# Kernel tuning notes

Hardware: AMD Instinct MI355X
Metric: run time of the kernel (lower is better)

## Reference

```python
import jax, jax.numpy as jnp
import numpy as np

SCALE_BASE = 512.0
GAMMA = 0.96875


def _rotate_every_two(x):
    x1 = x[..., ::2]
    x2 = x[..., 1::2]
    return jnp.stack([-x2, x1], axis=-1).reshape(x.shape)


def _dup_interleave(m):
    # [L, d/2] -> [L, d], each column duplicated: (a,b) -> (a,a,b,b)
    return jnp.repeat(m, 2, axis=-1)


def _xpos(x, downscale=False):
    # x: [B, L, d]; offset = 0 (parallel form)
    B, L, d = x.shape
    half = d // 2
    pos = jnp.arange(L, dtype=x.dtype)
    # xpos per-channel scale base
    sv = (jnp.arange(0, d, 2, dtype=x.dtype) + 0.4 * d) / (1.4 * d)   # [d/2]
    scale = sv[None, :] ** (pos[:, None] / SCALE_BASE)                 # [L, d/2]
    if downscale:
        scale = 1.0 / scale
    inv_freq = 1.0 / (10000.0 ** (jnp.arange(half, dtype=x.dtype) / half))
    sinusoid = pos[:, None] * inv_freq[None, :]                        # [L, d/2]
    sin = _dup_interleave(jnp.sin(sinusoid) * scale)                   # [L, d]
    cos = _dup_interleave(jnp.cos(sinusoid) * scale)                   # [L, d]
    return x * cos[None] + _rotate_every_two(x) * sin[None]


def _get_D(seq_len, dtype):
    idx = jnp.arange(seq_len)
    diff = idx[:, None] - idx[None, :]                                 # n - m
    safe = jnp.where(diff >= 0, diff, 0).astype(dtype)
    return jnp.where(diff >= 0, GAMMA ** safe, jnp.zeros((), dtype))   # [L, L]


def setup_inputs() -> dict:
    key = jax.random.key(0)
    k1, k2, k3, k4 = jax.random.split(key, 4)
    B, L, H, D = 2, 4096, 1024, 64
    X = jax.random.normal(k1, (B, L, H), dtype=jnp.float32)
    W_Q = jax.random.normal(k2, (H, D), dtype=jnp.float32) / H
    W_K = jax.random.normal(k3, (H, D), dtype=jnp.float32) / H
    W_V = jax.random.normal(k4, (H, D), dtype=jnp.float32) / H
    return {"X": X, "W_Q": W_Q, "W_K": W_K, "W_V": W_V}


def reference(X, W_Q, W_K, W_V):
    L = X.shape[1]
    Dmask = _get_D(L, X.dtype)                     # [L, L]
    Q = _xpos(X @ W_Q)                             # [B, L, d]
    K = _xpos(X @ W_K, downscale=True)             # [B, L, d]
    V = X @ W_V                                    # [B, L, v]
    ret = jnp.einsum('bnd,bmd->bnm', Q, K) * Dmask[None]  # [B, L, L]
    return ret @ V                                 # [B, L, v]
```

## Files before the change

### kernel.cpp

```cpp
#include <hip/hip_runtime.h>
#include <math.h>

#define NB 2
#define LL 4096
#define HH 1024
#define DD 64
#define CHK 64
#define NCH 64
#define BLROWS (NB*LL)
#define GAMMA 0.96875f

typedef _Float16 f16x8 __attribute__((ext_vector_type(8)));
typedef float    f32x4 __attribute__((ext_vector_type(4)));

#define WCH 12288

__global__ __launch_bounds__(256) void prep_w(
    const float* __restrict__ WQ, const float* __restrict__ WK,
    const float* __restrict__ WV, _Float16* __restrict__ Whg,
    _Float16* __restrict__ Wlg)
{
    const int g  = blockIdx.x * 256 + threadIdx.x;
    const int m  = g >> 14;
    const int km = g & 16383;
    const int k  = km >> 4;
    const int d4 = (km & 15) * 4;
    const float* Wm = (m == 0) ? WQ : (m == 1) ? WK : WV;
    const float4 w = *(const float4*)&Wm[(size_t)k * DD + d4];
    const float vals[4] = {w.x, w.y, w.z, w.w};
#pragma unroll
    for (int e = 0; e < 4; ++e) {
        const int n = m * 64 + d4 + e;
        const float x = vals[e] * 1024.f;
        const _Float16 h = (_Float16)x;
        const _Float16 l = (_Float16)(x - (float)h);
        const int off = (k >> 6) * WCH +
                        (((n >> 4) * 2 + ((k >> 5) & 1)) * 64 +
                         ((k >> 3) & 3) * 16 + (n & 15)) * 8 + (k & 7);
        Whg[off] = h;
        Wlg[off] = l;
    }
}

__global__ __launch_bounds__(256) void proj_mfma(
    const float* __restrict__ X, const _Float16* __restrict__ Whg,
    const _Float16* __restrict__ Wlg, float* __restrict__ Qx,
    float* __restrict__ Kx, float* __restrict__ Vx)
{
    __shared__ __align__(16) _Float16 lds[28672];
    _Float16* Xh = lds;
    _Float16* Xl = lds + 2048;
    _Float16* Wh = lds + 4096;
    _Float16* Wl = lds + 16384;

    const int tid  = threadIdx.x;
    const int wv   = tid >> 6;
    const int lane = tid & 63;
    const int r0   = blockIdx.x * 32;

    const int xrow = tid >> 3;
    const int xk8  = (tid & 7) * 8;
    const int xslot = (((xrow >> 4) * 2 + (xk8 >> 5)) * 64 +
                       ((xk8 >> 3) & 3) * 16 + (xrow & 15)) * 8;

    f32x4 acc[6];
#pragma unroll
    for (int i = 0; i < 6; ++i) acc[i] = (f32x4){0.f, 0.f, 0.f, 0.f};

    float4 pxa, pxb;
    f16x8  pwh[6], pwl[6];
    {
        const float* xp = &X[(size_t)(r0 + xrow) * HH + xk8];
        pxa = *(const float4*)&xp[0];
        pxb = *(const float4*)&xp[4];
#pragma unroll
        for (int i = 0; i < 6; ++i) {
            pwh[i] = *(const f16x8*)&Whg[(size_t)(tid + i * 256) * 8];
            pwl[i] = *(const f16x8*)&Wlg[(size_t)(tid + i * 256) * 8];
        }
    }

    for (int ch = 0; ch < 16; ++ch) {
        __syncthreads();
        {
            const float xv[8] = {pxa.x, pxa.y, pxa.z, pxa.w,
                                 pxb.x, pxb.y, pxb.z, pxb.w};
            f16x8 hv, lv;
#pragma unroll
            for (int e = 0; e < 8; ++e) {
                const _Float16 h = (_Float16)xv[e];
                hv[e] = h;
                lv[e] = (_Float16)(xv[e] - (float)h);
            }
            *(f16x8*)&Xh[xslot] = hv;
            *(f16x8*)&Xl[xslot] = lv;
#pragma unroll
            for (int i = 0; i < 6; ++i) {
                *(f16x8*)&Wh[(tid + i * 256) * 8] = pwh[i];
                *(f16x8*)&Wl[(tid + i * 256) * 8] = pwl[i];
            }
        }
        __syncthreads();
        if (ch + 1 < 16) {
            const float* xp = &X[(size_t)(r0 + xrow) * HH + (ch + 1) * 64 + xk8];
            pxa = *(const float4*)&xp[0];
            pxb = *(const float4*)&xp[4];
            const size_t cb = (size_t)(ch + 1) * WCH;
#pragma unroll
            for (int i = 0; i < 6; ++i) {
                pwh[i] = *(const f16x8*)&Whg[cb + (size_t)(tid + i * 256) * 8];
                pwl[i] = *(const f16x8*)&Wlg[cb + (size_t)(tid + i * 256) * 8];
            }
        }
#pragma unroll
        for (int kt = 0; kt < 2; ++kt) {
            const f16x8 a0h = *(const f16x8*)&Xh[((0 * 2 + kt) * 64 + lane) * 8];
            const f16x8 a0l = *(const f16x8*)&Xl[((0 * 2 + kt) * 64 + lane) * 8];
            const f16x8 a1h = *(const f16x8*)&Xh[((1 * 2 + kt) * 64 + lane) * 8];
            const f16x8 a1l = *(const f16x8*)&Xl[((1 * 2 + kt) * 64 + lane) * 8];
#pragma unroll
            for (int cj = 0; cj < 3; ++cj) {
                const int ctg = wv * 3 + cj;
                const f16x8 bh = *(const f16x8*)&Wh[((ctg * 2 + kt) * 64 + lane) * 8];
                const f16x8 bl = *(const f16x8*)&Wl[((ctg * 2 + kt) * 64 + lane) * 8];
                acc[cj] = __builtin_amdgcn_mfma_f32_16x16x32_f16(a0h, bh, acc[cj], 0, 0, 0);
                acc[cj] = __builtin_amdgcn_mfma_f32_16x16x32_f16(a0h, bl, acc[cj], 0, 0, 0);
                acc[cj] = __builtin_amdgcn_mfma_f32_16x16x32_f16(a0l, bh, acc[cj], 0, 0, 0);
                acc[3 + cj] = __builtin_amdgcn_mfma_f32_16x16x32_f16(a1h, bh, acc[3 + cj], 0, 0, 0);
                acc[3 + cj] = __builtin_amdgcn_mfma_f32_16x16x32_f16(a1h, bl, acc[3 + cj], 0, 0, 0);
                acc[3 + cj] = __builtin_amdgcn_mfma_f32_16x16x32_f16(a1l, bh, acc[3 + cj], 0, 0, 0);
            }
        }
    }

    const int quad = lane >> 4;
    const int c16  = lane & 15;
#pragma unroll
    for (int rt = 0; rt < 2; ++rt) {
#pragma unroll
        for (int cj = 0; cj < 3; ++cj) {
            const int ctg = wv * 3 + cj;
            const f32x4 v = acc[rt * 3 + cj];
            const int col = ctg * 16 + c16;
            const int mat = ctg >> 2;
            const int d   = col & 63;
            if (mat < 2) {
                const int i2 = d >> 1;
                const float sv   = (2.f * (float)i2 + 25.6f) / 89.6f;
                const float l2sv = log2f(sv);
                const float ifr  = exp2f(-13.28771237954945f * ((float)i2 / 32.f));
                const float sgn  = (mat == 0) ? 1.f : -1.f;
                float* dst = (mat == 0) ? Qx : Kx;
#pragma unroll
                for (int r = 0; r < 4; ++r) {
                    const int row = r0 + rt * 16 + quad * 4 + r;
                    const float val = v[r] * (1.f / 1024.f);
                    const float p = __shfl_xor(val, 1, 64);
                    const float pf = (float)(row & (LL - 1));
                    const float scl = exp2f(sgn * (pf * (1.f / 512.f)) * l2sv);
                    float s, c;
                    sincosf(pf * ifr, &s, &c);
                    s *= scl; c *= scl;
                    const float o = ((col & 1) == 0) ? val * c - p * s
                                                     : val * c + p * s;
                    dst[(size_t)row * DD + d] = o;
                }
            } else {
#pragma unroll
                for (int r = 0; r < 4; ++r) {
                    const int row = r0 + rt * 16 + quad * 4 + r;
                    Vx[(size_t)row * DD + d] = v[r] * (1.f / 1024.f);
                }
            }
        }
    }
}

__global__ __launch_bounds__(256) void chunk_kv(
    const float* __restrict__ Kx, const float* __restrict__ Vx,
    float* __restrict__ U)
{
    __shared__ float Kl[CHK][DD];
    __shared__ float Vl[CHK][32];
    const int tid   = threadIdx.x;
    const int bc    = blockIdx.x;
    const int chunk = bc >> 1;
    const int dph   = (bc & 1) * 32;
    const size_t base = (size_t)chunk * CHK * DD;
    const float l2g = log2f(GAMMA);
#pragma unroll
    for (int i = 0; i < 4; ++i) {
        const int f   = tid + i * 256;
        const int row = f >> 4;
        const int c4  = (f & 15) * 4;
        float4 kv = *(const float4*)&Kx[base + (size_t)row * DD + c4];
        const float w = exp2f((float)(CHK - 1 - row) * l2g);
        kv.x *= w; kv.y *= w; kv.z *= w; kv.w *= w;
        *(float4*)&Kl[row][c4] = kv;
    }
#pragma unroll
    for (int i = 0; i < 2; ++i) {
        const int f   = tid + i * 256;
        const int row = f >> 3;
        const int c4  = (f & 7) * 4;
        *(float4*)&Vl[row][c4] = *(const float4*)&Vx[base + (size_t)row * DD + dph + c4];
    }
    __syncthreads();
    const int dgr = tid >> 4;
    const int dc  = tid & 15;
    float a[4][2] = {{0,0},{0,0},{0,0},{0,0}};
#pragma unroll 8
    for (int j = 0; j < CHK; ++j) {
        const float4 kv = *(const float4*)&Kl[j][dgr * 4];
        const float2 vv = *(const float2*)&Vl[j][dc * 2];
        a[0][0] += kv.x * vv.x; a[0][1] += kv.x * vv.y;
        a[1][0] += kv.y * vv.x; a[1][1] += kv.y * vv.y;
        a[2][0] += kv.z * vv.x; a[2][1] += kv.z * vv.y;
        a[3][0] += kv.w * vv.x; a[3][1] += kv.w * vv.y;
    }
#pragma unroll
    for (int r = 0; r < 4; ++r) {
        *(float2*)&U[((size_t)chunk * DD + dgr * 4 + r) * DD + dph + dc * 2] =
            make_float2(a[r][0], a[r][1]);
    }
}

__global__ __launch_bounds__(256) void chunk_out(
    const float* __restrict__ Qx, const float* __restrict__ Kx,
    const float* __restrict__ Vx, const float* __restrict__ U,
    float* __restrict__ out)
{
    __shared__ __align__(16) float smA[6272];
    __shared__ __align__(16) float VTl[128 * 64];
    __shared__ float pwl[CHK + 1];
    const int tid   = threadIdx.x;
    const int bc    = blockIdx.x;
    const int chunk = bc >> 1;
    const int nh    = (bc & 1) * 32;
    const size_t base = (size_t)chunk * CHK * DD;

    if (tid <= CHK) pwl[tid] = exp2f((float)tid * log2f(GAMMA));

#pragma unroll
    for (int i = 0; i < 2; ++i) {
        const int f   = tid + i * 256;
        const int row = f >> 4;
        const int c4  = (f & 15) * 4;
        *(float4*)&smA[row * 68 + c4] =
            *(const float4*)&Qx[base + (size_t)(nh + row) * DD + c4];
    }
#pragma unroll
    for (int i = 0; i < 4; ++i) {
        const int f  = tid + i * 256;
        const int m  = f & 63;
        const int k4 = (f >> 6) * 4;
        const float4 kk = *(const float4*)&Kx[base + (size_t)m * DD + k4];
        smA[2176 + (k4 + 0) * 64 + m] = kk.x;
        smA[2176 + (k4 + 1) * 64 + m] = kk.y;
        smA[2176 + (k4 + 2) * 64 + m] = kk.z;
        smA[2176 + (k4 + 3) * 64 + m] = kk.w;
    }
#pragma unroll
    for (int i = 0; i < 4; ++i) {
        const int f   = tid + i * 256;
        const int row = f >> 4;
        const int c4  = (f & 15) * 4;
        *(float4*)&VTl[row * 64 + c4] =
            *(const float4*)&Vx[base + (size_t)row * DD + c4];
    }
    {
        const int cloc = chunk & 63;
        const float g64 = exp2f(64.f * log2f(GAMMA));
#pragma unroll
        for (int i = 0; i < 4; ++i) {
            const int f   = tid + i * 256;
            const int row = f >> 4;
            const int c4  = (f & 15) * 4;
            float tx = 0.f, ty = 0.f, tz = 0.f, tw = 0.f;
            float w = 1.f;
            for (int dl = 1; dl <= 8; ++dl) {
                if (dl <= cloc) {
                    const float4 u = *(const float4*)
                        &U[((size_t)(chunk - dl) * DD + row) * DD + c4];
                    tx += w * u.x; ty += w * u.y; tz += w * u.z; tw += w * u.w;
                }
                w *= g64;
            }
            *(float4*)&VTl[(64 + row) * 64 + c4] = make_float4(tx, ty, tz, tw);
        }
    }
    __syncthreads();

    const int ng = tid >> 4;
    const int mg = tid & 15;
    const int m0 = mg * 4;
    float sacc[2][4];
#pragma unroll
    for (int r = 0; r < 2; ++r)
#pragma unroll
        for (int j = 0; j < 4; ++j) sacc[r][j] = 0.f;

#pragma unroll 4
    for (int k4 = 0; k4 < 16; ++k4) {
        const float4 qv0 = *(const float4*)&smA[(ng * 2 + 0) * 68 + k4 * 4];
        const float4 qv1 = *(const float4*)&smA[(ng * 2 + 1) * 68 + k4 * 4];
#pragma unroll
        for (int u = 0; u < 4; ++u) {
            const float4 kv = *(const float4*)&smA[2176 + (k4 * 4 + u) * 64 + m0];
            const float x0 = (u == 0) ? qv0.x : (u == 1) ? qv0.y : (u == 2) ? qv0.z : qv0.w;
            const float x1 = (u == 0) ? qv1.x : (u == 1) ? qv1.y : (u == 2) ? qv1.z : qv1.w;
            sacc[0][0] += x0 * kv.x; sacc[0][1] += x0 * kv.y; sacc[0][2] += x0 * kv.z; sacc[0][3] += x0 * kv.w;
            sacc[1][0] += x1 * kv.x; sacc[1][1] += x1 * kv.y; sacc[1][2] += x1 * kv.z; sacc[1][3] += x1 * kv.w;
        }
    }
    const float4 qa0 = *(const float4*)&smA[(ng * 2 + 0) * 68 + m0];
    const float4 qa1 = *(const float4*)&smA[(ng * 2 + 1) * 68 + m0];
    __syncthreads();

#pragma unroll
    for (int r = 0; r < 2; ++r) {
        const int nl = ng * 2 + r;
        const int n  = nh + nl;
        float4 sv;
        sv.x = (n >= m0 + 0) ? sacc[r][0] * pwl[n - (m0 + 0)] : 0.f;
        sv.y = (n >= m0 + 1) ? sacc[r][1] * pwl[n - (m0 + 1)] : 0.f;
        sv.z = (n >= m0 + 2) ? sacc[r][2] * pwl[n - (m0 + 2)] : 0.f;
        sv.w = (n >= m0 + 3) ? sacc[r][3] * pwl[n - (m0 + 3)] : 0.f;
        *(float4*)&smA[nl * 132 + m0] = sv;
        const float w = pwl[n + 1];
        const float4 qa = r ? qa1 : qa0;
        *(float4*)&smA[nl * 132 + 64 + m0] =
            make_float4(qa.x * w, qa.y * w, qa.z * w, qa.w * w);
    }
    __syncthreads();

    const int dg = tid & 15;
    float oacc[2][4];
#pragma unroll
    for (int r = 0; r < 2; ++r)
#pragma unroll
        for (int j = 0; j < 4; ++j) oacc[r][j] = 0.f;

#pragma unroll 4
    for (int m4 = 0; m4 < 32; ++m4) {
        const float4 s0 = *(const float4*)&smA[(ng * 2 + 0) * 132 + m4 * 4];
        const float4 s1 = *(const float4*)&smA[(ng * 2 + 1) * 132 + m4 * 4];
#pragma unroll
        for (int mm = 0; mm < 4; ++mm) {
            const float4 vv = *(const float4*)&VTl[(m4 * 4 + mm) * 64 + dg * 4];
            const float a0 = (mm == 0) ? s0.x : (mm == 1) ? s0.y : (mm == 2) ? s0.z : s0.w;
            const float a1 = (mm == 0) ? s1.x : (mm == 1) ? s1.y : (mm == 2) ? s1.z : s1.w;
            oacc[0][0] += a0 * vv.x; oacc[0][1] += a0 * vv.y; oacc[0][2] += a0 * vv.z; oacc[0][3] += a0 * vv.w;
            oacc[1][0] += a1 * vv.x; oacc[1][1] += a1 * vv.y; oacc[1][2] += a1 * vv.z; oacc[1][3] += a1 * vv.w;
        }
    }
#pragma unroll
    for (int r = 0; r < 2; ++r) {
        *(float4*)&out[base + (size_t)(nh + ng * 2 + r) * DD + dg * 4] =
            make_float4(oacc[r][0], oacc[r][1], oacc[r][2], oacc[r][3]);
    }
}

extern "C" void kernel_launch(void* const* d_in, const int* in_sizes, int n_in,
                              void* d_out, int out_size, void* d_ws, size_t ws_size,
                              hipStream_t stream)
{
    const float* X  = (const float*)d_in[0];
    const float* WQ = (const float*)d_in[1];
    const float* WK = (const float*)d_in[2];
    const float* WV = (const float*)d_in[3];
    float* out = (float*)d_out;

    float* ws = (float*)d_ws;
    float* Qx = ws;
    float* Kx = Qx + (size_t)BLROWS * DD;
    float* Vx = Kx + (size_t)BLROWS * DD;
    float* U  = Vx + (size_t)BLROWS * DD;
    _Float16* Whg = (_Float16*)(U + (size_t)NB * NCH * DD * DD);
    _Float16* Wlg = Whg + 196608;

    hipLaunchKernelGGL(prep_w, dim3(192), dim3(256), 0, stream,
                       WQ, WK, WV, Whg, Wlg);
    hipLaunchKernelGGL(proj_mfma, dim3(BLROWS / 32), dim3(256), 0, stream,
                       X, Whg, Wlg, Qx, Kx, Vx);
    hipLaunchKernelGGL(chunk_kv, dim3(2 * NB * NCH), dim3(256), 0, stream, Kx, Vx, U);
    hipLaunchKernelGGL(chunk_out, dim3(2 * NB * NCH), dim3(256), 0, stream,
                       Qx, Kx, Vx, U, out);
}
```

Baseline: 124.3 us.

## Store Q/K/V as fp16 with chunk-relative xpos scaling and MFMA chunk attention

Projections now write Q, K and V in fp16, and the xpos scale is taken relative to the row's position inside its 64-row chunk, with the inter-chunk scale folded into the state-combination factors. This halves intermediate traffic and avoids fp16 overflow. A new prep_vt kernel combines the decayed U states and lays out V and the state into MFMA B-fragment order. chunk_out now uses fp16 MFMA for both QK^T and SV instead of scalar FMA. The weight prep writes directly in fragment order with vector stores. The changes add an extra launch and lower precision, which risks tolerance failures.

```diff
diff --git a/kernel.cpp b/kernel.cpp
--- a/kernel.cpp
+++ b/kernel.cpp
@@ -8,9 +8,11 @@
 #define CHK 64
 #define NCH 64
 #define BLROWS (NB*LL)
+#define NCHT (NB*NCH)
 #define GAMMA 0.96875f
 
 typedef _Float16 f16x8 __attribute__((ext_vector_type(8)));
+typedef _Float16 f16x4 __attribute__((ext_vector_type(4)));
 typedef float    f32x4 __attribute__((ext_vector_type(4)));
 
 #define WCH 12288
@@ -20,32 +22,35 @@
     const float* __restrict__ WV, _Float16* __restrict__ Whg,
     _Float16* __restrict__ Wlg)
 {
-    const int g  = blockIdx.x * 256 + threadIdx.x;
-    const int m  = g >> 14;
-    const int km = g & 16383;
-    const int k  = km >> 4;
-    const int d4 = (km & 15) * 4;
+    const unsigned t = blockIdx.x * 256 + threadIdx.x;
+    const unsigned kchunk = t / 1536u;
+    const unsigned s = t - kchunk * 1536u;
+    const int ct2  = s >> 6;
+    const int lane = s & 63;
+    const int n16  = ct2 >> 1;
+    const int kt   = ct2 & 1;
+    const int quad = lane >> 4;
+    const int n    = n16 * 16 + (lane & 15);
+    const int k0   = (int)kchunk * 64 + kt * 32 + quad * 8;
+    const int m    = n >> 6;
+    const int d    = n & 63;
     const float* Wm = (m == 0) ? WQ : (m == 1) ? WK : WV;
-    const float4 w = *(const float4*)&Wm[(size_t)k * DD + d4];
-    const float vals[4] = {w.x, w.y, w.z, w.w};
-#pragma unroll
-    for (int e = 0; e < 4; ++e) {
-        const int n = m * 64 + d4 + e;
-        const float x = vals[e] * 1024.f;
+    f16x8 hv, lv;
+#pragma unroll
+    for (int j = 0; j < 8; ++j) {
+        const float x = Wm[(size_t)(k0 + j) * DD + d] * 1024.f;
         const _Float16 h = (_Float16)x;
-        const _Float16 l = (_Float16)(x - (float)h);
-        const int off = (k >> 6) * WCH +
-                        (((n >> 4) * 2 + ((k >> 5) & 1)) * 64 +
-                         ((k >> 3) & 3) * 16 + (n & 15)) * 8 + (k & 7);
-        Whg[off] = h;
-        Wlg[off] = l;
-    }
+        hv[j] = h;
+        lv[j] = (_Float16)(x - (float)h);
+    }
+    *(f16x8*)&Whg[(size_t)t * 8] = hv;
+    *(f16x8*)&Wlg[(size_t)t * 8] = lv;
 }
 
 __global__ __launch_bounds__(256) void proj_mfma(
     const float* __restrict__ X, const _Float16* __restrict__ Whg,
-    const _Float16* __restrict__ Wlg, float* __restrict__ Qx,
-    float* __restrict__ Kx, float* __restrict__ Vx)
+    const _Float16* __restrict__ Wlg, _Float16* __restrict__ Qr,
+    _Float16* __restrict__ Kr, _Float16* __restrict__ Vr)
 {
     __shared__ __align__(16) _Float16 lds[28672];
     _Float16* Xh = lds;
@@ -150,26 +155,27 @@
                 const float l2sv = log2f(sv);
                 const float ifr  = exp2f(-13.28771237954945f * ((float)i2 / 32.f));
                 const float sgn  = (mat == 0) ? 1.f : -1.f;
-                float* dst = (mat == 0) ? Qx : Kx;
+                _Float16* dst = (mat == 0) ? Qr : Kr;
 #pragma unroll
                 for (int r = 0; r < 4; ++r) {
                     const int row = r0 + rt * 16 + quad * 4 + r;
                     const float val = v[r] * (1.f / 1024.f);
                     const float p = __shfl_xor(val, 1, 64);
-                    const float pf = (float)(row & (LL - 1));
-                    const float scl = exp2f(sgn * (pf * (1.f / 512.f)) * l2sv);
+                    const float pf  = (float)(row & (LL - 1));
+                    const float pfs = (float)(row & 63);
+                    const float scl = exp2f(sgn * (pfs * (1.f / 512.f)) * l2sv);
                     float s, c;
                     sincosf(pf * ifr, &s, &c);
                     s *= scl; c *= scl;
                     const float o = ((col & 1) == 0) ? val * c - p * s
                                                      : val * c + p * s;
-                    dst[(size_t)row * DD + d] = o;
+                    dst[(size_t)row * DD + d] = (_Float16)o;
                 }
             } else {
 #pragma unroll
                 for (int r = 0; r < 4; ++r) {
                     const int row = r0 + rt * 16 + quad * 4 + r;
-                    Vx[(size_t)row * DD + d] = v[r] * (1.f / 1024.f);
+                    Vr[(size_t)row * DD + d] = (_Float16)(v[r] * (1.f / 1024.f));
                 }
             }
         }
@@ -177,33 +183,27 @@
 }
 
 __global__ __launch_bounds__(256) void chunk_kv(
-    const float* __restrict__ Kx, const float* __restrict__ Vx,
+    const _Float16* __restrict__ Kr, const _Float16* __restrict__ Vr,
     float* __restrict__ U)
 {
-    __shared__ float Kl[CHK][DD];
-    __shared__ float Vl[CHK][32];
+    __shared__ _Float16 Kl[64 * 64];
+    __shared__ _Float16 Vl[64 * 32];
+    __shared__ float pwd[64];
     const int tid   = threadIdx.x;
     const int bc    = blockIdx.x;
     const int chunk = bc >> 1;
     const int dph   = (bc & 1) * 32;
-    const size_t base = (size_t)chunk * CHK * DD;
+    const size_t rbase = (size_t)chunk * CHK * DD;
     const float l2g = log2f(GAMMA);
-#pragma unroll
-    for (int i = 0; i < 4; ++i) {
-        const int f   = tid + i * 256;
-        const int row = f >> 4;
-        const int c4  = (f & 15) * 4;
-        float4 kv = *(const float4*)&Kx[base + (size_t)row * DD + c4];
-        const float w = exp2f((float)(CHK - 1 - row) * l2g);
-        kv.x *= w; kv.y *= w; kv.z *= w; kv.w *= w;
-        *(float4*)&Kl[row][c4] = kv;
-    }
-#pragma unroll
-    for (int i = 0; i < 2; ++i) {
-        const int f   = tid + i * 256;
-        const int row = f >> 3;
-        const int c4  = (f & 7) * 4;
-        *(float4*)&Vl[row][c4] = *(const float4*)&Vx[base + (size_t)row * DD + dph + c4];
+
+    if (tid < 64) pwd[tid] = exp2f((float)(63 - tid) * l2g);
+    {
+        const int row = tid >> 2;
+        const int c0  = (tid & 3) * 16;
+        *(f16x8*)&Kl[row * 64 + c0]     = *(const f16x8*)&Kr[rbase + (size_t)row * DD + c0];
+        *(f16x8*)&Kl[row * 64 + c0 + 8] = *(const f16x8*)&Kr[rbase + (size_t)row * DD + c0 + 8];
+        const int c1 = (tid & 3) * 8;
+        *(f16x8*)&Vl[row * 32 + c1] = *(const f16x8*)&Vr[rbase + (size_t)row * DD + dph + c1];
     }
     __syncthreads();
     const int dgr = tid >> 4;
@@ -211,12 +211,16 @@
     float a[4][2] = {{0,0},{0,0},{0,0},{0,0}};
 #pragma unroll 8
     for (int j = 0; j < CHK; ++j) {
-        const float4 kv = *(const float4*)&Kl[j][dgr * 4];
-        const float2 vv = *(const float2*)&Vl[j][dc * 2];
-        a[0][0] += kv.x * vv.x; a[0][1] += kv.x * vv.y;
-        a[1][0] += kv.y * vv.x; a[1][1] += kv.y * vv.y;
-        a[2][0] += kv.z * vv.x; a[2][1] += kv.z * vv.y;
-        a[3][0] += kv.w * vv.x; a[3][1] += kv.w * vv.y;
+        const f16x4 kh = *(const f16x4*)&Kl[j * 64 + dgr * 4];
+        const float w  = pwd[j];
+        const float v0 = (float)Vl[j * 32 + dc * 2]     * w;
+        const float v1 = (float)Vl[j * 32 + dc * 2 + 1] * w;
+        const float k0 = (float)kh[0], k1 = (float)kh[1];
+        const float k2 = (float)kh[2], k3 = (float)kh[3];
+        a[0][0] += k0 * v0; a[0][1] += k0 * v1;
+        a[1][0] += k1 * v0; a[1][1] += k1 * v1;
+        a[2][0] += k2 * v0; a[2][1] += k2 * v1;
+        a[3][0] += k3 * v0; a[3][1] += k3 * v1;
     }
 #pragma unroll
     for (int r = 0; r < 4; ++r) {
@@ -225,140 +229,152 @@
     }
 }
 
+__global__ __launch_bounds__(256) void prep_vt(
+    const _Float16* __restrict__ Vr, const float* __restrict__ U,
+    _Float16* __restrict__ VTf)
+{
+    __shared__ float    Tl[64 * 68];
+    __shared__ _Float16 Vl[64 * 72];
+    const int tid   = threadIdx.x;
+    const int chunk = blockIdx.x;
+    const int cloc  = chunk & 63;
+    const size_t rbase = (size_t)chunk * CHK * DD;
+    const float l2g = log2f(GAMMA);
+
+    {
+        const int row = tid >> 2;
+        const int c0  = (tid & 3) * 16;
+        *(f16x8*)&Vl[row * 72 + c0]     = *(const f16x8*)&Vr[rbase + (size_t)row * DD + c0];
+        *(f16x8*)&Vl[row * 72 + c0 + 8] = *(const f16x8*)&Vr[rbase + (size_t)row * DD + c0 + 8];
+    }
+    {
+        const int d  = tid >> 2;
+        const int dq = (tid & 3) * 16;
+        const float sv = (2.f * (float)(d >> 1) + 25.6f) / 89.6f;
+        const float l2sv = log2f(sv);
+        float acc[16];
+#pragma unroll
+        for (int i = 0; i < 16; ++i) acc[i] = 0.f;
+        for (int dl = 1; dl <= 8; ++dl) {
+            if (dl <= cloc) {
+                const float f = exp2f(64.f * (float)(dl - 1) * l2g +
+                                      0.125f * (float)dl * l2sv);
+                const float* up = &U[((size_t)(chunk - dl) * DD + d) * DD + dq];
+#pragma unroll
+                for (int i4 = 0; i4 < 4; ++i4) {
+                    const float4 u = *(const float4*)&up[i4 * 4];
+                    acc[i4 * 4 + 0] += f * u.x; acc[i4 * 4 + 1] += f * u.y;
+                    acc[i4 * 4 + 2] += f * u.z; acc[i4 * 4 + 3] += f * u.w;
+                }
+            }
+        }
+#pragma unroll
+        for (int i = 0; i < 16; ++i) Tl[d * 68 + dq + i] = acc[i];
+    }
+    __syncthreads();
+#pragma unroll
+    for (int it = 0; it < 4; ++it) {
+        const int s    = tid + it * 256;
+        const int nt   = s >> 8;
+        const int ks   = (s >> 6) & 3;
+        const int lane = s & 63;
+        const int quad = lane >> 4;
+        const int dp   = nt * 16 + (lane & 15);
+        const int mb   = ks * 32 + quad * 8;
+        f16x8 v;
+#pragma unroll
+        for (int j = 0; j < 8; ++j) {
+            const int mrow = mb + j;
+            v[j] = (mrow < 64) ? Vl[mrow * 72 + dp]
+                               : (_Float16)Tl[(mrow - 64) * 68 + dp];
+        }
+        *(f16x8*)&VTf[(size_t)chunk * 8192 + (size_t)s * 8] = v;
+    }
+}
+
 __global__ __launch_bounds__(256) void chunk_out(
-    const float* __restrict__ Qx, const float* __restrict__ Kx,
-    const float* __restrict__ Vx, const float* __restrict__ U,
-    float* __restrict__ out)
-{
-    __shared__ __align__(16) float smA[6272];
-    __shared__ __align__(16) float VTl[128 * 64];
-    __shared__ float pwl[CHK + 1];
+    const _Float16* __restrict__ Qr, const _Float16* __restrict__ Kr,
+    const _Float16* __restrict__ VTf, float* __restrict__ out)
+{
+    __shared__ _Float16 Sb[32 * 136];
+    __shared__ float pwl[65];
     const int tid   = threadIdx.x;
     const int bc    = blockIdx.x;
     const int chunk = bc >> 1;
     const int nh    = (bc & 1) * 32;
-    const size_t base = (size_t)chunk * CHK * DD;
-
-    if (tid <= CHK) pwl[tid] = exp2f((float)tid * log2f(GAMMA));
-
-#pragma unroll
-    for (int i = 0; i < 2; ++i) {
-        const int f   = tid + i * 256;
-        const int row = f >> 4;
-        const int c4  = (f & 15) * 4;
-        *(float4*)&smA[row * 68 + c4] =
-            *(const float4*)&Qx[base + (size_t)(nh + row) * DD + c4];
-    }
-#pragma unroll
-    for (int i = 0; i < 4; ++i) {
-        const int f  = tid + i * 256;
-        const int m  = f & 63;
-        const int k4 = (f >> 6) * 4;
-        const float4 kk = *(const float4*)&Kx[base + (size_t)m * DD + k4];
-        smA[2176 + (k4 + 0) * 64 + m] = kk.x;
-        smA[2176 + (k4 + 1) * 64 + m] = kk.y;
-        smA[2176 + (k4 + 2) * 64 + m] = kk.z;
-        smA[2176 + (k4 + 3) * 64 + m] = kk.w;
-    }
-#pragma unroll
-    for (int i = 0; i < 4; ++i) {
-        const int f   = tid + i * 256;
-        const int row = f >> 4;
-        const int c4  = (f & 15) * 4;
-        *(float4*)&VTl[row * 64 + c4] =
-            *(const float4*)&Vx[base + (size_t)row * DD + c4];
-    }
-    {
-        const int cloc = chunk & 63;
-        const float g64 = exp2f(64.f * log2f(GAMMA));
-#pragma unroll
-        for (int i = 0; i < 4; ++i) {
-            const int f   = tid + i * 256;
-            const int row = f >> 4;
-            const int c4  = (f & 15) * 4;
-            float tx = 0.f, ty = 0.f, tz = 0.f, tw = 0.f;
-            float w = 1.f;
-            for (int dl = 1; dl <= 8; ++dl) {
-                if (dl <= cloc) {
-                    const float4 u = *(const float4*)
-                        &U[((size_t)(chunk - dl) * DD + row) * DD + c4];
-                    tx += w * u.x; ty += w * u.y; tz += w * u.z; tw += w * u.w;
-                }
-                w *= g64;
-            }
-            *(float4*)&VTl[(64 + row) * 64 + c4] = make_float4(tx, ty, tz, tw);
-        }
-    }
+    const int w     = tid >> 6;
+    const int lane  = tid & 63;
+    const int quad  = lane >> 4;
+    const int l15   = lane & 15;
+    const int mtile = w >> 1;
+    const int npair = (w & 1) * 2;
+    const size_t rowbase = (size_t)chunk * CHK + nh;
+
+    if (tid < 65) pwl[tid] = exp2f((float)tid * log2f(GAMMA));
+
+    f16x8 aQ[2], bK[2][2];
+#pragma unroll
+    for (int ks = 0; ks < 2; ++ks)
+        aQ[ks] = *(const f16x8*)&Qr[(rowbase + mtile * 16 + l15) * DD +
+                                    ks * 32 + quad * 8];
+#pragma unroll
+    for (int nt = 0; nt < 2; ++nt)
+#pragma unroll
+        for (int ks = 0; ks < 2; ++ks)
+            bK[nt][ks] = *(const f16x8*)&Kr[((size_t)chunk * CHK +
+                                            (npair + nt) * 16 + l15) * DD +
+                                            ks * 32 + quad * 8];
     __syncthreads();
 
-    const int ng = tid >> 4;
-    const int mg = tid & 15;
-    const int m0 = mg * 4;
-    float sacc[2][4];
-#pragma unroll
-    for (int r = 0; r < 2; ++r)
-#pragma unroll
-        for (int j = 0; j < 4; ++j) sacc[r][j] = 0.f;
-
-#pragma unroll 4
-    for (int k4 = 0; k4 < 16; ++k4) {
-        const float4 qv0 = *(const float4*)&smA[(ng * 2 + 0) * 68 + k4 * 4];
-        const float4 qv1 = *(const float4*)&smA[(ng * 2 + 1) * 68 + k4 * 4];
-#pragma unroll
-        for (int u = 0; u < 4; ++u) {
-            const float4 kv = *(const float4*)&smA[2176 + (k4 * 4 + u) * 64 + m0];
-            const float x0 = (u == 0) ? qv0.x : (u == 1) ? qv0.y : (u == 2) ? qv0.z : qv0.w;
-            const float x1 = (u == 0) ? qv1.x : (u == 1) ? qv1.y : (u == 2) ? qv1.z : qv1.w;
-            sacc[0][0] += x0 * kv.x; sacc[0][1] += x0 * kv.y; sacc[0][2] += x0 * kv.z; sacc[0][3] += x0 * kv.w;
-            sacc[1][0] += x1 * kv.x; sacc[1][1] += x1 * kv.y; sacc[1][2] += x1 * kv.z; sacc[1][3] += x1 * kv.w;
-        }
-    }
-    const float4 qa0 = *(const float4*)&smA[(ng * 2 + 0) * 68 + m0];
-    const float4 qa1 = *(const float4*)&smA[(ng * 2 + 1) * 68 + m0];
+    f32x4 sA[2] = {(f32x4){0.f,0.f,0.f,0.f}, (f32x4){0.f,0.f,0.f,0.f}};
+#pragma unroll
+    for (int nt = 0; nt < 2; ++nt)
+#pragma unroll
+        for (int ks = 0; ks < 2; ++ks)
+            sA[nt] = __builtin_amdgcn_mfma_f32_16x16x32_f16(aQ[ks], bK[nt][ks],
+                                                            sA[nt], 0, 0, 0);
+#pragma unroll
+    for (int nt = 0; nt < 2; ++nt) {
+        const int m = (npair + nt) * 16 + l15;
+#pragma unroll
+        for (int r = 0; r < 4; ++r) {
+            const int nl = mtile * 16 + quad * 4 + r;
+            const int n64 = nh + nl;
+            const float val = (n64 >= m) ? sA[nt][r] * pwl[n64 - m] : 0.f;
+            Sb[nl * 136 + m] = (_Float16)val;
+        }
+    }
+    if ((w & 1) == 0) {
+        const float g = pwl[nh + mtile * 16 + l15 + 1];
+#pragma unroll
+        for (int ks = 0; ks < 2; ++ks) {
+            f16x8 qv;
+#pragma unroll
+            for (int j = 0; j < 8; ++j)
+                qv[j] = (_Float16)((float)aQ[ks][j] * g);
+            *(f16x8*)&Sb[(mtile * 16 + l15) * 136 + 64 + ks * 32 + quad * 8] = qv;
+        }
+    }
     __syncthreads();
 
-#pragma unroll
-    for (int r = 0; r < 2; ++r) {
-        const int nl = ng * 2 + r;
-        const int n  = nh + nl;
-        float4 sv;
-        sv.x = (n >= m0 + 0) ? sacc[r][0] * pwl[n - (m0 + 0)] : 0.f;
-        sv.y = (n >= m0 + 1) ? sacc[r][1] * pwl[n - (m0 + 1)] : 0.f;
-        sv.z = (n >= m0 + 2) ? sacc[r][2] * pwl[n - (m0 + 2)] : 0.f;
-        sv.w = (n >= m0 + 3) ? sacc[r][3] * pwl[n - (m0 + 3)] : 0.f;
-        *(float4*)&smA[nl * 132 + m0] = sv;
-        const float w = pwl[n + 1];
-        const float4 qa = r ? qa1 : qa0;
-        *(float4*)&smA[nl * 132 + 64 + m0] =
-            make_float4(qa.x * w, qa.y * w, qa.z * w, qa.w * w);
-    }
-    __syncthreads();
-
-    const int dg = tid & 15;
-    float oacc[2][4];
-#pragma unroll
-    for (int r = 0; r < 2; ++r)
-#pragma unroll
-        for (int j = 0; j < 4; ++j) oacc[r][j] = 0.f;
-
-#pragma unroll 4
-    for (int m4 = 0; m4 < 32; ++m4) {
-        const float4 s0 = *(const float4*)&smA[(ng * 2 + 0) * 132 + m4 * 4];
-        const float4 s1 = *(const float4*)&smA[(ng * 2 + 1) * 132 + m4 * 4];
-#pragma unroll
-        for (int mm = 0; mm < 4; ++mm) {
-            const float4 vv = *(const float4*)&VTl[(m4 * 4 + mm) * 64 + dg * 4];
-            const float a0 = (mm == 0) ? s0.x : (mm == 1) ? s0.y : (mm == 2) ? s0.z : s0.w;
-            const float a1 = (mm == 0) ? s1.x : (mm == 1) ? s1.y : (mm == 2) ? s1.z : s1.w;
-            oacc[0][0] += a0 * vv.x; oacc[0][1] += a0 * vv.y; oacc[0][2] += a0 * vv.z; oacc[0][3] += a0 * vv.w;
-            oacc[1][0] += a1 * vv.x; oacc[1][1] += a1 * vv.y; oacc[1][2] += a1 * vv.z; oacc[1][3] += a1 * vv.w;
-        }
-    }
-#pragma unroll
-    for (int r = 0; r < 2; ++r) {
-        *(float4*)&out[base + (size_t)(nh + ng * 2 + r) * DD + dg * 4] =
-            make_float4(oacc[r][0], oacc[r][1], oacc[r][2], oacc[r][3]);
-    }
+    f32x4 oA[2] = {(f32x4){0.f,0.f,0.f,0.f}, (f32x4){0.f,0.f,0.f,0.f}};
+#pragma unroll
+    for (int ks = 0; ks < 4; ++ks) {
+        const f16x8 aS = *(const f16x8*)&Sb[(mtile * 16 + l15) * 136 +
+                                            ks * 32 + quad * 8];
+#pragma unroll
+        for (int nt = 0; nt < 2; ++nt) {
+            const f16x8 bV = *(const f16x8*)&VTf[(size_t)chunk * 8192 +
+                (size_t)((((npair + nt) * 4 + ks) * 64 + lane)) * 8];
+            oA[nt] = __builtin_amdgcn_mfma_f32_16x16x32_f16(aS, bV, oA[nt], 0, 0, 0);
+        }
+    }
+#pragma unroll
+    for (int nt = 0; nt < 2; ++nt)
+#pragma unroll
+        for (int r = 0; r < 4; ++r)
+            out[(rowbase + mtile * 16 + quad * 4 + r) * DD +
+                (npair + nt) * 16 + l15] = oA[nt][r];
 }
 
 extern "C" void kernel_launch(void* const* d_in, const int* in_sizes, int n_in,
@@ -371,19 +387,20 @@
     const float* WV = (const float*)d_in[3];
     float* out = (float*)d_out;
 
-    float* ws = (float*)d_ws;
-    float* Qx = ws;
-    float* Kx = Qx + (size_t)BLROWS * DD;
-    float* Vx = Kx + (size_t)BLROWS * DD;
-    float* U  = Vx + (size_t)BLROWS * DD;
-    _Float16* Whg = (_Float16*)(U + (size_t)NB * NCH * DD * DD);
+    _Float16* Whg = (_Float16*)d_ws;
     _Float16* Wlg = Whg + 196608;
-
-    hipLaunchKernelGGL(prep_w, dim3(192), dim3(256), 0, stream,
+    _Float16* Qr  = Wlg + 196608;
+    _Float16* Kr  = Qr + (size_t)BLROWS * DD;
+    _Float16* Vr  = Kr + (size_t)BLROWS * DD;
+    _Float16* VTf = Vr + (size_t)BLROWS * DD;
+    float*    U   = (float*)(VTf + (size_t)NCHT * 8192);
+
+    hipLaunchKernelGGL(prep_w, dim3(96), dim3(256), 0, stream,
                        WQ, WK, WV, Whg, Wlg);
     hipLaunchKernelGGL(proj_mfma, dim3(BLROWS / 32), dim3(256), 0, stream,
-                       X, Whg, Wlg, Qx, Kx, Vx);
-    hipLaunchKernelGGL(chunk_kv, dim3(2 * NB * NCH), dim3(256), 0, stream, Kx, Vx, U);
-    hipLaunchKernelGGL(chunk_out, dim3(2 * NB * NCH), dim3(256), 0, stream,
-                       Qx, Kx, Vx, U, out);
-}
+                       X, Whg, Wlg, Qr, Kr, Vr);
+    hipLaunchKernelGGL(chunk_kv, dim3(2 * NCHT), dim3(256), 0, stream, Kr, Vr, U);
+    hipLaunchKernelGGL(prep_vt, dim3(NCHT), dim3(256), 0, stream, Vr, U, VTf);
+    hipLaunchKernelGGL(chunk_out, dim3(2 * NCHT), dim3(256), 0, stream,
+                       Qr, Kr, VTf, out);
+}
```

Measured after the change: 116.9 us. -5.9%, faster.
